# Kernel optimization log

Measured on AMD Instinct MI355X. Metric: run time of the kernel, lower is better.

Reference implementation:

```python
import jax, jax.numpy as jnp
import numpy as np

B, N, DIM = 16, 4096, 1024   # batch, n_out query tokens, embedding dim
T, E = 8, 64                 # n_tasks (readout heads), per-task output channels


def setup_inputs() -> dict:
    key = jax.random.key(0)
    k1, k2, k3, k4 = jax.random.split(key, 4)
    output_embs = jax.random.normal(k1, (B, N, DIM), dtype=jnp.float32)
    output_readout_index = jax.random.randint(k2, (B, N), 0, T, dtype=jnp.int64)
    # Stacked per-task nn.Linear(dim, E) weights/biases (torch Linear: y = x @ W.T + b)
    bound = 1.0 / np.sqrt(DIM)
    W = jax.random.uniform(k3, (T, DIM, E), minval=-bound, maxval=bound, dtype=jnp.float32)
    b = jax.random.uniform(k4, (T, E), minval=-bound, maxval=bound, dtype=jnp.float32)
    return {"output_embs": output_embs, "output_readout_index": output_readout_index,
            "W": W, "b": b}


def reference(output_embs, output_readout_index, W, b):
    """Per-token head-selected linear readout.

    Equivalent to the torch module's per-task mask/gather/Linear loop: every
    token t with output_readout_index==k gets projections[k](emb_t). The torch
    version concatenates selected rows into a dict per task; here we keep the
    rows in dense token order [B, N, E] (same values, fixed shapes for jit).
    """
    # All-head projection: [B, N, T, E]
    all_out = jnp.einsum('bnd,tde->bnte', output_embs, W) + b
    # Select each token's assigned head
    idx = output_readout_index[..., None, None]          # [B, N, 1, 1]
    out = jnp.take_along_axis(all_out, idx, axis=2)[:, :, 0, :]  # [B, N, E]
    return out
```

## Files before the change

kernel.cpp:

```cpp
#include <hip/hip_runtime.h>
#include <hip/hip_bf16.h>

#define NTOK  65536
#define DIM_  1024
#define NHEAD 8
#define EOUT  64
#define KBLK  32
#define CNT_STRIDE 32

typedef __bf16 bf16x8 __attribute__((ext_vector_type(8)));
typedef float  f32x4  __attribute__((ext_vector_type(4)));
typedef unsigned short u16x8 __attribute__((ext_vector_type(8)));

__device__ inline __bf16 cvt_bf16(float f) {
    __hip_bfloat16 h = __float2bfloat16(f);
    return __builtin_bit_cast(__bf16, h);
}

__device__ inline void gload_lds16(const void* g, void* lds) {
    __builtin_amdgcn_global_load_lds(
        (const __attribute__((address_space(1))) unsigned int*)g,
        (__attribute__((address_space(3))) unsigned int*)lds,
        16, 0, 0);
}

__global__ __launch_bounds__(256) void pack_and_bucket(
    const float* __restrict__ W, const int* __restrict__ idx,
    unsigned short* __restrict__ Wp, int* __restrict__ cnt,
    int* __restrict__ list)
{
    int x = blockIdx.x * blockDim.x + threadIdx.x;
    {
        int j  = x & 7;
        int l  = (x >> 3) & 63;
        int et = (x >> 9) & 3;
        int kb = (x >> 11) & 31;
        int t  = x >> 16;
        int k = kb * 32 + (l >> 4) * 8 + j;
        int e = et * 16 + (l & 15);
        float v = W[((size_t)t * DIM_ + k) * EOUT + e];
        __hip_bfloat16 h = __float2bfloat16(v);
        Wp[x] = __builtin_bit_cast(unsigned short, h);
    }

    if (blockIdx.x < NTOK / 1024) {
        int wave = threadIdx.x >> 6;
        int lane = threadIdx.x & 63;
        int gw   = blockIdx.x * 4 + wave;
        int tbase = gw * 256;
        int t[4];
        #pragma unroll
        for (int c = 0; c < 4; ++c) t[c] = idx[tbase + c * 64 + lane];

        #pragma unroll
        for (int h = 0; h < NHEAD; ++h) {
            unsigned long long m[4];
            int nh = 0;
            #pragma unroll
            for (int c = 0; c < 4; ++c) {
                m[c] = __ballot(t[c] == h);
                nh += __popcll(m[c]);
            }
            int base = 0;
            if (lane == 0 && nh) base = atomicAdd(&cnt[h * CNT_STRIDE], nh);
            base = __shfl(base, 0, 64);
            int pre = 0;
            #pragma unroll
            for (int c = 0; c < 4; ++c) {
                if (t[c] == h) {
                    int rank = __popcll(m[c] & ((1ull << lane) - 1ull));
                    list[h * NTOK + base + pre + rank] = tbase + c * 64 + lane;
                }
                pre += __popcll(m[c]);
            }
        }
    }
}

__global__ __launch_bounds__(256, 4) void readout_gemm(
    const float* __restrict__ emb, const float* __restrict__ bias,
    const int* __restrict__ cnt, const int* __restrict__ list,
    const unsigned short* __restrict__ Wp, float* __restrict__ out)
{
    __shared__ __align__(16) char smem[4 * 8192];

    int g = blockIdx.x;
    int head = -1, tile = 0, count = 0, total = 0;
    #pragma unroll
    for (int h = 0; h < NHEAD; ++h) {
        int c = cnt[h * CNT_STRIDE];
        int th = (c + 31) >> 5;
        if (head < 0 && g < total + th) { head = h; tile = g - total; count = c; }
        total += th;
    }
    if (head < 0) return;

    int wave = threadIdx.x >> 6;
    int lane = threadIdx.x & 63;
    int quad = lane >> 4, l16 = lane & 15;
    int rg = wave >> 1;
    int ep = wave & 1;
    int eb = ep * 2;

    const int* mylist = list + head * NTOK;
    int mbase = tile * 32;

    int srow0 = wave * 8 + quad;
    int srow1 = srow0 + 4;
    int sm0 = mbase + srow0; if (sm0 > count - 1) sm0 = count - 1;
    int sm1 = mbase + srow1; if (sm1 > count - 1) sm1 = count - 1;
    const char* gs0 = (const char*)(emb + (size_t)mylist[sm0] * DIM_)
                      + ((l16 ^ (srow0 & 15)) * 16);
    const char* gs1 = (const char*)(emb + (size_t)mylist[sm1] * DIM_)
                      + ((l16 ^ (srow1 & 15)) * 16);
    char* ldsw = smem + wave * 2048;

    int arow = rg * 16 + l16;

    const u16x8* wp = reinterpret_cast<const u16x8*>(Wp + (size_t)head * 65536);

    u16x8 BA[2][2], BB[2][2];
    #pragma unroll
    for (int kk = 0; kk < 2; ++kk)
        #pragma unroll
        for (int e = 0; e < 2; ++e)
            BA[kk][e] = wp[(kk * 4 + eb + e) * 64 + lane];

    #pragma unroll
    for (int s = 0; s < 3; ++s) {
        char* d = ldsw + s * 8192;
        gload_lds16(gs0 + s * 256, d);
        gload_lds16(gs1 + s * 256, d + 1024);
    }

    f32x4 acc[2] = {};

    auto body = [&](int c, u16x8 (&Bc)[2][2], u16x8 (&Bn)[2][2]) {
        if (c + 1 < 16) {
            #pragma unroll
            for (int kk = 0; kk < 2; ++kk)
                #pragma unroll
                for (int e = 0; e < 2; ++e)
                    Bn[kk][e] = wp[((2 * (c + 1) + kk) * 4 + eb + e) * 64 + lane];
        }
        asm volatile("s_waitcnt lgkmcnt(0)" ::: "memory");
        __builtin_amdgcn_s_barrier();
        if (c + 3 < 16) {
            char* d = ldsw + ((c + 3) & 3) * 8192;
            gload_lds16(gs0 + (c + 3) * 256, d);
            gload_lds16(gs1 + (c + 3) * 256, d + 1024);
        }
        if (c < 13)       asm volatile("s_waitcnt vmcnt(8)" ::: "memory");
        else if (c == 13) asm volatile("s_waitcnt vmcnt(6)" ::: "memory");
        else if (c == 14) asm volatile("s_waitcnt vmcnt(4)" ::: "memory");
        else              asm volatile("s_waitcnt vmcnt(0)" ::: "memory");
        __builtin_amdgcn_s_barrier();

        const char* bb = smem + (c & 3) * 8192 + arow * 256;
        #pragma unroll
        for (int kk = 0; kk < 2; ++kk) {
            int cu0 = kk * 8 + quad * 2;
            f32x4 lo = *(const f32x4*)(bb + (((cu0 + 0) ^ l16) * 16));
            f32x4 hi = *(const f32x4*)(bb + (((cu0 + 1) ^ l16) * 16));
            bf16x8 a;
            #pragma unroll
            for (int j = 0; j < 4; ++j) {
                a[j]     = cvt_bf16(lo[j]);
                a[j + 4] = cvt_bf16(hi[j]);
            }
            #pragma unroll
            for (int e = 0; e < 2; ++e)
                acc[e] = __builtin_amdgcn_mfma_f32_16x16x32_bf16(
                    a, __builtin_bit_cast(bf16x8, Bc[kk][e]), acc[e], 0, 0, 0);
        }
    };

    #pragma unroll 8
    for (int c = 0; c < 16; c += 2) {
        body(c,     BA, BB);
        body(c + 1, BB, BA);
    }

    int tok[4];
    #pragma unroll
    for (int i = 0; i < 4; ++i) {
        int m = mbase + rg * 16 + quad * 4 + i;
        tok[i] = (m < count) ? mylist[m] : -1;
    }
    #pragma unroll
    for (int e = 0; e < 2; ++e) {
        float bv = bias[head * EOUT + (eb + e) * 16 + l16];
        #pragma unroll
        for (int i = 0; i < 4; ++i)
            if (tok[i] >= 0)
                __builtin_nontemporal_store(acc[e][i] + bv,
                    &out[(size_t)tok[i] * EOUT + (eb + e) * 16 + l16]);
    }
}

extern "C" void kernel_launch(void* const* d_in, const int* in_sizes, int n_in,
                              void* d_out, int out_size, void* d_ws, size_t ws_size,
                              hipStream_t stream) {
    const float* emb  = (const float*)d_in[0];
    const int*   idx  = (const int*)d_in[1];
    const float* W    = (const float*)d_in[2];
    const float* bias = (const float*)d_in[3];
    float* out = (float*)d_out;

    char* ws = (char*)d_ws;
    int* cnt  = (int*)ws;
    int* list = (int*)(ws + 1024);
    unsigned short* Wp = (unsigned short*)(ws + 1024 + (size_t)NHEAD * NTOK * sizeof(int));

    (void)hipMemsetAsync(cnt, 0, NHEAD * CNT_STRIDE * sizeof(int), stream);
    pack_and_bucket<<<(NHEAD * KBLK * 4 * 64 * 8) / 256, 256, 0, stream>>>(W, idx, Wp, cnt, list);
    readout_gemm<<<2055, 256, 0, stream>>>(emb, bias, cnt, list, Wp, out);
}
```

Measured before the change: 400.0 us.

## Stage larger K chunks in LDS with triple buffering and inline weight loads

Each LDS stage now covers 128 fp32 K values per row (512 B), so there are 8 chunks instead of 16. A 3-buffer ring with prefetch distance 2 replaces the 4-buffer ring with distance 3. The register double-buffering of the bf16 weight fragments is dropped, and weights are now loaded inside the k-loop just before use. Occupancy drops from 4 to 3 blocks per CU because LDS grows from 32KB to 48KB; this trades fewer barriers and waitcnt round trips for less latency hiding.

```diff
diff --git a/kernel.cpp b/kernel.cpp
--- a/kernel.cpp
+++ b/kernel.cpp
@@ -7,6 +7,11 @@
 #define EOUT  64
 #define KBLK  32
 #define CNT_STRIDE 32
+
+#define CH_ROWB   512
+#define CH_LDS    (32 * CH_ROWB)
+#define NCHUNK    8
+#define NBUF      3
 
 typedef __bf16 bf16x8 __attribute__((ext_vector_type(8)));
 typedef float  f32x4  __attribute__((ext_vector_type(4)));
@@ -77,12 +82,12 @@
     }
 }
 
-__global__ __launch_bounds__(256, 4) void readout_gemm(
+__global__ __launch_bounds__(256, 3) void readout_gemm(
     const float* __restrict__ emb, const float* __restrict__ bias,
     const int* __restrict__ cnt, const int* __restrict__ list,
     const unsigned short* __restrict__ Wp, float* __restrict__ out)
 {
-    __shared__ __align__(16) char smem[4 * 8192];
+    __shared__ __align__(16) char smem[NBUF * CH_LDS];
 
     int g = blockIdx.x;
     int head = -1, tile = 0, count = 0, total = 0;
@@ -105,80 +110,65 @@
     const int* mylist = list + head * NTOK;
     int mbase = tile * 32;
 
-    int srow0 = wave * 8 + quad;
-    int srow1 = srow0 + 4;
-    int sm0 = mbase + srow0; if (sm0 > count - 1) sm0 = count - 1;
-    int sm1 = mbase + srow1; if (sm1 > count - 1) sm1 = count - 1;
-    const char* gs0 = (const char*)(emb + (size_t)mylist[sm0] * DIM_)
-                      + ((l16 ^ (srow0 & 15)) * 16);
-    const char* gs1 = (const char*)(emb + (size_t)mylist[sm1] * DIM_)
-                      + ((l16 ^ (srow1 & 15)) * 16);
-    char* ldsw = smem + wave * 2048;
+    const char* gsrc[4];
+    int u31 = lane & 31;
+    #pragma unroll
+    for (int i = 0; i < 4; ++i) {
+        int row = wave * 8 + i * 2 + (lane >> 5);
+        int m = mbase + row; if (m > count - 1) m = count - 1;
+        gsrc[i] = (const char*)(emb + (size_t)mylist[m] * DIM_)
+                  + ((u31 ^ (row & 15)) * 16);
+    }
+    char* ldsw = smem + (wave * 8) * CH_ROWB;
 
     int arow = rg * 16 + l16;
 
     const u16x8* wp = reinterpret_cast<const u16x8*>(Wp + (size_t)head * 65536);
 
-    u16x8 BA[2][2], BB[2][2];
-    #pragma unroll
-    for (int kk = 0; kk < 2; ++kk)
-        #pragma unroll
-        for (int e = 0; e < 2; ++e)
-            BA[kk][e] = wp[(kk * 4 + eb + e) * 64 + lane];
-
-    #pragma unroll
-    for (int s = 0; s < 3; ++s) {
-        char* d = ldsw + s * 8192;
-        gload_lds16(gs0 + s * 256, d);
-        gload_lds16(gs1 + s * 256, d + 1024);
+    #pragma unroll
+    for (int s = 0; s < 2; ++s) {
+        char* d = ldsw + s * CH_LDS;
+        #pragma unroll
+        for (int i = 0; i < 4; ++i)
+            gload_lds16(gsrc[i] + s * CH_ROWB, d + i * 1024);
     }
 
     f32x4 acc[2] = {};
 
-    auto body = [&](int c, u16x8 (&Bc)[2][2], u16x8 (&Bn)[2][2]) {
-        if (c + 1 < 16) {
-            #pragma unroll
-            for (int kk = 0; kk < 2; ++kk)
-                #pragma unroll
-                for (int e = 0; e < 2; ++e)
-                    Bn[kk][e] = wp[((2 * (c + 1) + kk) * 4 + eb + e) * 64 + lane];
-        }
+    #pragma unroll
+    for (int c = 0; c < NCHUNK; ++c) {
         asm volatile("s_waitcnt lgkmcnt(0)" ::: "memory");
         __builtin_amdgcn_s_barrier();
-        if (c + 3 < 16) {
-            char* d = ldsw + ((c + 3) & 3) * 8192;
-            gload_lds16(gs0 + (c + 3) * 256, d);
-            gload_lds16(gs1 + (c + 3) * 256, d + 1024);
+        if (c + 2 < NCHUNK) {
+            char* d = ldsw + ((c + 2) % NBUF) * CH_LDS;
+            #pragma unroll
+            for (int i = 0; i < 4; ++i)
+                gload_lds16(gsrc[i] + (c + 2) * CH_ROWB, d + i * 1024);
         }
-        if (c < 13)       asm volatile("s_waitcnt vmcnt(8)" ::: "memory");
-        else if (c == 13) asm volatile("s_waitcnt vmcnt(6)" ::: "memory");
-        else if (c == 14) asm volatile("s_waitcnt vmcnt(4)" ::: "memory");
-        else              asm volatile("s_waitcnt vmcnt(0)" ::: "memory");
+        if (c < NCHUNK - 2)       asm volatile("s_waitcnt vmcnt(8)" ::: "memory");
+        else if (c == NCHUNK - 2) asm volatile("s_waitcnt vmcnt(4)" ::: "memory");
+        else                      asm volatile("s_waitcnt vmcnt(0)" ::: "memory");
         __builtin_amdgcn_s_barrier();
 
-        const char* bb = smem + (c & 3) * 8192 + arow * 256;
-        #pragma unroll
-        for (int kk = 0; kk < 2; ++kk) {
-            int cu0 = kk * 8 + quad * 2;
-            f32x4 lo = *(const f32x4*)(bb + (((cu0 + 0) ^ l16) * 16));
-            f32x4 hi = *(const f32x4*)(bb + (((cu0 + 1) ^ l16) * 16));
+        const char* bb = smem + (c % NBUF) * CH_LDS + arow * CH_ROWB;
+        #pragma unroll
+        for (int kb = 0; kb < 4; ++kb) {
+            int u0 = kb * 8 + quad * 2;
+            f32x4 lo = *(const f32x4*)(bb + (((u0 + 0) ^ l16) * 16));
+            f32x4 hi = *(const f32x4*)(bb + (((u0 + 1) ^ l16) * 16));
+            u16x8 b0 = wp[((c * 4 + kb) * 4 + eb + 0) * 64 + lane];
+            u16x8 b1 = wp[((c * 4 + kb) * 4 + eb + 1) * 64 + lane];
             bf16x8 a;
             #pragma unroll
             for (int j = 0; j < 4; ++j) {
                 a[j]     = cvt_bf16(lo[j]);
                 a[j + 4] = cvt_bf16(hi[j]);
             }
-            #pragma unroll
-            for (int e = 0; e < 2; ++e)
-                acc[e] = __builtin_amdgcn_mfma_f32_16x16x32_bf16(
-                    a, __builtin_bit_cast(bf16x8, Bc[kk][e]), acc[e], 0, 0, 0);
+            acc[0] = __builtin_amdgcn_mfma_f32_16x16x32_bf16(
+                a, __builtin_bit_cast(bf16x8, b0), acc[0], 0, 0, 0);
+            acc[1] = __builtin_amdgcn_mfma_f32_16x16x32_bf16(
+                a, __builtin_bit_cast(bf16x8, b1), acc[1], 0, 0, 0);
         }
-    };
-
-    #pragma unroll 8
-    for (int c = 0; c < 16; c += 2) {
-        body(c,     BA, BB);
-        body(c + 1, BB, BA);
     }
 
     int tok[4];
```

Measured after the change: 406.0 us. Within noise of the previous version (+1.5%).
